# Performance work log

Hardware: AMD Instinct MI355X
Metric: run time of the kernel (lower is better)

## Reference

```python
import jax, jax.numpy as jnp
import numpy as np

BS, NV, BASE_NF = 1, 6890, 13776
NF = 2 * BASE_NF            # fill_back duplicates faces with reversed winding
TS = 3                      # tex_size
IS = 256                    # image_size
NEAR, FAR = 0.1, 100.0
VIEW_ANGLE = 30.0
EYE = np.array([0.0, 0.0, -(1.0 / np.tan(np.radians(VIEW_ANGLE)) + 1.0)], dtype=np.float32)
BG = np.zeros(3, np.float32)               # background_color
AMB_INT, DIR_INT = 1.0, 0.0                # default light settings
AMB_COLOR = np.ones(3, np.float32)
DIR_COLOR = np.ones(3, np.float32)
LIGHT_DIR = np.array([0.0, 1.0, 0.0], np.float32)


def setup_inputs():
    key = jax.random.key(0)
    k1, k2, k3, k4, k5 = jax.random.split(key, 5)
    cam = jnp.concatenate([0.8 + 0.4 * jax.random.uniform(k1, (BS, 1)),
                           0.4 * (jax.random.uniform(k2, (BS, 2)) - 0.5)], axis=-1)
    vertices = 0.5 * jax.random.normal(k3, (BS, NV, 3), dtype=jnp.float32)
    uv_imgs = jax.random.uniform(k4, (BS, 3, IS, IS), dtype=jnp.float32)
    f0 = jax.random.randint(k5, (BASE_NF, 3), 0, NV, dtype=jnp.int32)
    faces = jnp.concatenate([f0, f0[:, ::-1]], axis=0)   # fill_back
    return {"cam": cam, "vertices": vertices, "uv_imgs": uv_imgs, "faces": faces}


def create_coords(ts):
    step = 1.0 / (ts - 1)
    ab = jnp.arange(ts, dtype=jnp.float32) * step
    xv, yv = jnp.meshgrid(ab, ab, indexing='ij')
    return jnp.stack([xv.ravel(), yv.ravel()], axis=0)   # [2, ts*ts]


def grid_sample_bilinear(img, grid):
    # img [B,C,H,W]; grid [B,N,2] with (x,y) in [-1,1]; align_corners=True
    B, C, H, W = img.shape
    x = (grid[..., 0] + 1.0) * 0.5 * (W - 1)
    y = (grid[..., 1] + 1.0) * 0.5 * (H - 1)
    x0 = jnp.floor(x); y0 = jnp.floor(y)
    wx = x - x0; wy = y - y0
    x0i = jnp.clip(x0, 0, W - 1).astype(jnp.int32)
    x1i = jnp.clip(x0 + 1, 0, W - 1).astype(jnp.int32)
    y0i = jnp.clip(y0, 0, H - 1).astype(jnp.int32)
    y1i = jnp.clip(y0 + 1, 0, H - 1).astype(jnp.int32)
    flat = img.reshape(B, C, H * W)
    def g(yi, xi):
        return jnp.take_along_axis(flat, (yi * W + xi)[:, None, :], axis=2)  # [B,C,N]
    return (g(y0i, x0i) * ((1 - wx) * (1 - wy))[:, None]
          + g(y0i, x1i) * (wx * (1 - wy))[:, None]
          + g(y1i, x0i) * ((1 - wx) * wy)[:, None]
          + g(y1i, x1i) * (wx * wy)[:, None])


def dynamic_sampler(cam, vertices, faces, coords):
    # batch_orth_proj_idrot -> points_to_faces -> points_to_sampler
    pts = cam[:, None, 0:1] * (vertices[:, :, :2] + cam[:, None, 1:])  # [B,NV,2]
    fpts = pts[:, faces]                                               # [B,NF,3,2]
    v2 = fpts[:, :, 2]
    m = jnp.stack([fpts[:, :, 0] - v2, fpts[:, :, 1] - v2], axis=-1)   # [B,NF,2,2]
    s = jnp.einsum('bfxk,kt->bfxt', m, coords) + v2[..., None]         # [B,NF,2,T2]
    s = jnp.transpose(s, (0, 1, 3, 2))                                 # [B,NF,T2,2]
    return jnp.clip(s, -1.0, 1.0)


def extract_tex(uv_imgs, sampler):
    B, nf, t2, _ = sampler.shape
    tex = grid_sample_bilinear(uv_imgs, sampler.reshape(B, nf * t2, 2))  # [B,3,NF*T2]
    tex = tex.reshape(B, 3, nf, TS, TS)
    tex = jnp.transpose(tex, (0, 2, 3, 4, 1))                            # [B,NF,T,T,3]
    return jnp.broadcast_to(tex[:, :, :, :, None, :], (B, nf, TS, TS, TS, 3))


def lighting(face_verts, textures):
    v10 = face_verts[:, :, 0] - face_verts[:, :, 1]
    v12 = face_verts[:, :, 2] - face_verts[:, :, 1]
    n = jnp.cross(v10, v12)
    n = n / jnp.maximum(jnp.linalg.norm(n, axis=-1, keepdims=True), 1e-5)
    cos = jnp.maximum(jnp.einsum('bfk,k->bf', n, jnp.asarray(LIGHT_DIR)), 0.0)
    light = AMB_INT * jnp.asarray(AMB_COLOR) + DIR_INT * cos[..., None] * jnp.asarray(DIR_COLOR)
    return textures * light[:, :, None, None, None, :]


def look_at(vertices):
    eye = jnp.asarray(EYE)
    up = jnp.array([0.0, 1.0, 0.0], jnp.float32)
    z = -eye / jnp.linalg.norm(eye)            # at = origin
    x = jnp.cross(up, z); x = x / jnp.linalg.norm(x)
    y = jnp.cross(z, x); y = y / jnp.linalg.norm(y)
    R = jnp.stack([x, y, z], axis=0)
    return (vertices - eye) @ R.T


def rasterize(face_verts, textures):
    # face_verts [B,NF,3,3]: screen x,y in [-1,1], z = depth. textures [B,NF,T,T,T,3].
    B, nf = face_verts.shape[:2]
    fx, fy, fz = face_verts[..., 0], face_verts[..., 1], face_verts[..., 2]
    x0, x1, x2 = fx[..., 0], fx[..., 1], fx[..., 2]
    y0, y1, y2 = fy[..., 0], fy[..., 1], fy[..., 2]
    a = jnp.stack([y1 - y2, y2 - y0, y0 - y1], -1)
    b = jnp.stack([x2 - x1, x0 - x2, x1 - x0], -1)
    c = jnp.stack([x1 * y2 - x2 * y1, x2 * y0 - x0 * y2, x0 * y1 - x1 * y0], -1)
    det = c.sum(-1)
    front = det > 0                                  # backface cull (fill_back handles both sides)
    det_safe = jnp.where(jnp.abs(det) > 1e-10, det, 1e-10)
    fz_safe = jnp.where(jnp.abs(fz) > 1e-6, fz, 1e-6)
    inv_z = 1.0 / fz_safe
    tex_flat = textures.reshape(B, nf * TS * TS * TS, 3)
    xp = (2.0 * jnp.arange(IS, dtype=jnp.float32) + 1.0 - IS) / IS
    yps = (2.0 * jnp.arange(IS, dtype=jnp.float32) + 1.0 - IS) / IS
    bg = jnp.asarray(BG)

    def row_fn(yp):
        # barycentric weights of every pixel in this row against every face
        w = (xp[None, :, None, None] * a[:, None] + yp * b[:, None] + c[:, None]) / det_safe[:, None, :, None]
        inside = (w.min(-1) >= 0.0) & (w.max(-1) <= 1.0) & front[:, None, :]
        den = jnp.sum(w * inv_z[:, None], -1)
        zp = jnp.where(den > 1e-8, 1.0 / jnp.maximum(den, 1e-8), FAR)
        valid = inside & (zp > NEAR) & (zp < FAR)
        depth = jnp.where(valid, zp, FAR)
        fidx = jnp.argmin(depth, axis=2)                                              # [B,W]
        hit = jnp.take_along_axis(depth, fidx[:, :, None], axis=2)[..., 0] < FAR
        w_sel = jnp.take_along_axis(w, fidx[:, :, None, None], axis=2)[:, :, 0, :]    # [B,W,3]
        z_sel = jnp.take_along_axis(fz_safe, fidx[:, :, None], axis=1)                # [B,W,3]
        wc = w_sel / z_sel                                                            # perspective-correct
        wc = wc / jnp.maximum(wc.sum(-1, keepdims=True), 1e-8)
        pos = jnp.clip(wc, 0.0, 1.0) * (TS - 1)
        lo_f = jnp.clip(jnp.floor(pos), 0, TS - 1)
        frac = pos - lo_f
        lo = lo_f.astype(jnp.int32)
        hi = jnp.minimum(lo + 1, TS - 1)
        color = jnp.zeros(w_sel.shape[:2] + (3,), jnp.float32)
        for bits in range(8):                         # trilinear sample of the TxTxT texture cube
            idx = fidx
            wgt = jnp.ones(w_sel.shape[:2], jnp.float32)
            for k in range(3):
                use_hi = (bits >> k) & 1
                ik = hi[..., k] if use_hi else lo[..., k]
                wgt = wgt * (frac[..., k] if use_hi else (1.0 - frac[..., k]))
                idx = idx * TS + ik
            cols = jnp.take_along_axis(tex_flat, idx[:, :, None], axis=1)             # [B,W,3]
            color = color + wgt[..., None] * cols
        return jnp.where(hit[..., None], color, bg)

    row_fn = jax.checkpoint(row_fn)
    def body(carry, yp):
        return carry, row_fn(yp)
    _, rows = jax.lax.scan(body, 0, yps)              # [H,B,W,3]
    return jnp.transpose(rows, (1, 3, 0, 2))          # [B,3,H,W]


def reference(cam, vertices, uv_imgs, faces):
    coords = create_coords(TS)
    sampler = dynamic_sampler(cam, vertices, faces, coords)
    textures = extract_tex(uv_imgs, sampler)
    textures = lighting(vertices[:, faces], textures)
    # orthographic projection (keep z), flip y, then look_at camera transform
    sc = cam[:, 0][:, None, None]
    tr = cam[:, 1:3][:, None, :]
    proj_xy = sc * (vertices[:, :, :2] + tr)
    proj = jnp.concatenate([proj_xy[..., :1], -proj_xy[..., 1:2], vertices[:, :, 2:]], axis=-1)
    v_cam = look_at(proj)
    images = rasterize(v_cam[:, faces], textures)
    return images, textures
```

## Files before the change

kernel.cpp:

```cpp
#include <hip/hip_runtime.h>
#include <hip/hip_bf16.h>

typedef unsigned long long u64;

static constexpr int NF = 27552;
static constexpr int IMGOFF = 3 * 256 * 256;
static constexpr int CAPMAX = 6144;
static constexpr int NWAVES = 8192;

#define EYEZ 2.7320508075688772f

static constexpr size_t OFF_KEYS  = 0;
static constexpr size_t OFF_QTOT  = 524288;
static constexpr size_t OFF_FCNT  = 524292;
static constexpr size_t OFF_CNT   = 524352;
static constexpr size_t OFF_CMETA = 532608;
static constexpr size_t OFF_CF    = 2105472;
static constexpr size_t OFF_CBB   = 3868800;
static constexpr size_t OFF_PXY   = 4309632;
static constexpr size_t OFF_LIST  = 5191296;

static constexpr u64 FARKEY = ((u64)0x42C80000u << 32);

__global__ __launch_bounds__(256) void face_prep(
    const float* __restrict__ cam,
    const float* __restrict__ verts,
    const int* __restrict__ faces,
    u64* __restrict__ keys,
    float* __restrict__ cf,
    float4* __restrict__ cbb,
    float* __restrict__ pxy,
    int* __restrict__ fcnt)
{
    int i = blockIdx.x * 256 + threadIdx.x;
    keys[i] = FARKEY;
    int f = i;
    if (f >= NF) return;
    float c0 = cam[0], c1 = cam[1], c2 = cam[2];
    float z3 = __fdiv_rn(EYEZ, __fsqrt_rn(__fmul_rn(EYEZ, EYEZ)));
    float x0r = __fdiv_rn(z3, __fsqrt_rn(__fmul_rn(z3, z3)));
    float wyy = __fmul_rn(z3, x0r);
    float y1r = __fdiv_rn(wyy, __fsqrt_rn(__fmul_rn(wyy, wyy)));

    float xs[3], ys[3], zs[3], pxv[3], pyv[3];
#pragma unroll
    for (int k = 0; k < 3; k++) {
        int vi = faces[f * 3 + k];
        float vx = verts[vi * 3 + 0];
        float vy = verts[vi * 3 + 1];
        float vz = verts[vi * 3 + 2];
        float px = __fmul_rn(c0, __fadd_rn(vx, c1));
        float py = __fmul_rn(c0, __fadd_rn(vy, c2));
        pxv[k] = px; pyv[k] = py;
        xs[k] = __fmul_rn(px, x0r);
        ys[k] = __fmul_rn(-py, y1r);
        zs[k] = __fmul_rn(__fadd_rn(vz, EYEZ), z3);
    }
    float* pp = pxy + (size_t)f * 8;
    *(float4*)pp = make_float4(pxv[0], pyv[0], pxv[1], pyv[1]);
    *(float2*)(pp + 4) = make_float2(pxv[2], pyv[2]);

    float a0 = __fsub_rn(ys[1], ys[2]);
    float a1 = __fsub_rn(ys[2], ys[0]);
    float a2 = __fsub_rn(ys[0], ys[1]);
    float b0 = __fsub_rn(xs[2], xs[1]);
    float b1 = __fsub_rn(xs[0], xs[2]);
    float b2 = __fsub_rn(xs[1], xs[0]);
    float cc0 = __fsub_rn(__fmul_rn(xs[1], ys[2]), __fmul_rn(xs[2], ys[1]));
    float cc1 = __fsub_rn(__fmul_rn(xs[2], ys[0]), __fmul_rn(xs[0], ys[2]));
    float cc2 = __fsub_rn(__fmul_rn(xs[0], ys[1]), __fmul_rn(xs[1], ys[0]));
    float det = __fadd_rn(__fadd_rn(cc0, cc1), cc2);
    if (det <= 0.0f) return;
    float ds  = (fabsf(det) > 1e-10f) ? det : 1e-10f;
    float z0 = (fabsf(zs[0]) > 1e-6f) ? zs[0] : 1e-6f;
    float z1 = (fabsf(zs[1]) > 1e-6f) ? zs[1] : 1e-6f;
    float z2 = (fabsf(zs[2]) > 1e-6f) ? zs[2] : 1e-6f;
    float iz0 = __fdiv_rn(1.0f, z0);
    float iz1 = __fdiv_rn(1.0f, z1);
    float iz2 = __fdiv_rn(1.0f, z2);

    int pos = atomicAdd(fcnt, 1);
    float* q = cf + (size_t)pos * 16;
    q[0] = a0; q[1] = a1; q[2] = a2;
    q[3] = b0; q[4] = b1; q[5] = b2;
    q[6] = cc0; q[7] = cc1; q[8] = cc2;
    q[9] = ds;
    q[10] = iz0; q[11] = iz1; q[12] = iz2;
    q[13] = 2e-6f * ((iz0 + iz1) + iz2) + 1e-7f;
    q[14] = __int_as_float(f);
    q[15] = fmaxf(fmaxf(iz0, iz1), iz2) * 1.0001f + 1e-7f;

    float4 bb;
    bb.x = fminf(fminf(xs[0], xs[1]), xs[2]) - 1e-4f;
    bb.y = fmaxf(fmaxf(xs[0], xs[1]), xs[2]) + 1e-4f;
    bb.z = fminf(fminf(ys[0], ys[1]), ys[2]) - 1e-4f;
    bb.w = fmaxf(fmaxf(ys[0], ys[1]), ys[2]) + 1e-4f;
    cbb[pos] = bb;
}

__global__ __launch_bounds__(256) void tex_sample(
    const float* __restrict__ pxy,
    const float* __restrict__ uv,
    float* __restrict__ out_tex)
{
    int id = blockIdx.x * 256 + threadIdx.x;
    if (id >= NF * 9) return;
    int f = id / 9, t = id - f * 9;
    const float* pp = pxy + (size_t)f * 8;
    float4 pA = *(const float4*)pp;
    float2 pB = *(const float2*)(pp + 4);
    float px[3] = {pA.x, pA.z, pB.x};
    float py[3] = {pA.y, pA.w, pB.y};
    const float abv[3] = {0.0f, 0.5f, 1.0f};
    int t1 = t / 3, t2 = t - t1 * 3;
    float uu = abv[t1], vv = abv[t2];
    float sx = __fadd_rn(__fadd_rn(__fmul_rn(__fsub_rn(px[0], px[2]), uu),
                                   __fmul_rn(__fsub_rn(px[1], px[2]), vv)), px[2]);
    float sy = __fadd_rn(__fadd_rn(__fmul_rn(__fsub_rn(py[0], py[2]), uu),
                                   __fmul_rn(__fsub_rn(py[1], py[2]), vv)), py[2]);
    sx = fminf(fmaxf(sx, -1.0f), 1.0f);
    sy = fminf(fmaxf(sy, -1.0f), 1.0f);
    float xg = __fmul_rn(__fmul_rn(__fadd_rn(sx, 1.0f), 0.5f), 255.0f);
    float yg = __fmul_rn(__fmul_rn(__fadd_rn(sy, 1.0f), 0.5f), 255.0f);
    float x0f = floorf(xg), y0f = floorf(yg);
    float wx = __fsub_rn(xg, x0f), wy = __fsub_rn(yg, y0f);
    int x0 = (int)x0f; x0 = x0 < 0 ? 0 : (x0 > 255 ? 255 : x0);
    int y0 = (int)y0f; y0 = y0 < 0 ? 0 : (y0 > 255 ? 255 : y0);
    int x1 = x0 + 1 > 255 ? 255 : x0 + 1;
    int y1 = y0 + 1 > 255 ? 255 : y0 + 1;
    float omwx = __fsub_rn(1.0f, wx), omwy = __fsub_rn(1.0f, wy);
    float w00 = __fmul_rn(omwx, omwy);
    float w10 = __fmul_rn(wx, omwy);
    float w01 = __fmul_rn(omwx, wy);
    float w11 = __fmul_rn(wx, wy);
    size_t tb = (size_t)f * 81 + (size_t)t1 * 27 + (size_t)t2 * 9;
#pragma unroll
    for (int c = 0; c < 3; c++) {
        const float* img = uv + c * 65536;
        float g00 = img[y0 * 256 + x0];
        float g10 = img[y0 * 256 + x1];
        float g01 = img[y1 * 256 + x0];
        float g11 = img[y1 * 256 + x1];
        float val = __fmul_rn(g00, w00);
        val = __fadd_rn(val, __fmul_rn(g10, w10));
        val = __fadd_rn(val, __fmul_rn(g01, w01));
        val = __fadd_rn(val, __fmul_rn(g11, w11));
        out_tex[tb + 0 + c] = val;
        out_tex[tb + 3 + c] = val;
        out_tex[tb + 6 + c] = val;
    }
}

__global__ __launch_bounds__(256, 8) void bin_faces(
    const float* __restrict__ cf,
    const float4* __restrict__ cbb,
    const int* __restrict__ fcnt,
    int* __restrict__ cnt,
    int* __restrict__ list,
    int cap)
{
    __shared__ int sfid[4][64];
    const int lane = threadIdx.x & 63;
    const int wid  = threadIdx.x >> 6;
    const int w = blockIdx.x * 4 + wid;
    const int jy = w / 431;
    const int p  = (w - jy * 431) * 64 + lane;
    const int n = *fcnt;
    const float ylo = (float)(16 * jy + 1 - 256) * (1.0f / 256.0f);
    const float yhi = (float)(16 * jy + 15 - 256) * (1.0f / 256.0f);

    bool rv = (p < n);
    float A0 = 0, A1 = 0, A2 = 0, B0 = 0, B1 = 0, B2 = 0;
    int jx0 = 32, jx1 = -1;
    if (rv) {
        float4 bb = cbb[p];
        rv = (yhi >= bb.z) && (ylo <= bb.w);
        if (rv) {
            const float4* q = (const float4*)(cf + (size_t)p * 16);
            float4 q0 = q[0], q1 = q[1], q2 = q[2];
            float a0 = q0.x, a1 = q0.y, a2 = q0.z;
            float b0 = q0.w, b1 = q1.x, b2 = q1.y;
            float c0 = q1.z, c1 = q1.w, c2 = q2.x;
            float K0 = fmaxf(b0 * ylo, b0 * yhi) + c0;
            float K1 = fmaxf(b1 * ylo, b1 * yhi) + c1;
            float K2 = fmaxf(b2 * ylo, b2 * yhi) + c2;
            A0 = a0 * (1.0f / 16.0f);
            A1 = a1 * (1.0f / 16.0f);
            A2 = a2 * (1.0f / 16.0f);
            B0 = a0 * (((a0 > 0.f ? 15.f : 1.f) - 256.f) * (1.0f / 256.0f)) + K0;
            B1 = a1 * (((a1 > 0.f ? 15.f : 1.f) - 256.f) * (1.0f / 256.0f)) + K1;
            B2 = a2 * (((a2 > 0.f ? 15.f : 1.f) - 256.f) * (1.0f / 256.0f)) + K2;
            jx0 = (int)floorf(16.0f * bb.x + 15.0625f);
            jx1 = (int)floorf(16.0f * bb.y + 15.9375f) + 1;
            jx0 = jx0 < 0 ? 0 : jx0;
            jx1 = jx1 > 31 ? 31 : jx1;
        }
    }
    if (__ballot(rv) == 0ull) return;

    sfid[wid][lane] = p;
    asm volatile("s_waitcnt lgkmcnt(0)" ::: "memory");

    u64 mymask = 0;
    for (int jx = 0; jx < 32; jx++) {
        float jf = (float)jx;
        bool pass = rv && (jx >= jx0) && (jx <= jx1) &&
                    (fmaf(jf, A0, B0) >= -1e-3f) &&
                    (fmaf(jf, A1, B1) >= -1e-3f) &&
                    (fmaf(jf, A2, B2) >= -1e-3f);
        u64 mk = __ballot(pass);
        if (lane == jx) mymask = mk;
    }

    int nadd = (lane < 32) ? __popcll(mymask) : 0;
    if (nadd == 0) return;
    int base = atomicAdd(&cnt[jy * 32 + lane], nadd);

    int* dst = list + (size_t)(jy * 32 + lane) * cap;
    u64 mm = mymask;
    int k = 0;
    while (mm) {
        int b = __builtin_ctzll(mm);
        mm &= mm - 1;
        int fid = sfid[wid][b];
        int pos = base + k;
        if (pos < cap) dst[pos] = fid;
        k++;
    }
}

__global__ __launch_bounds__(1024) void prefix_chunks(
    const int* __restrict__ cnt,
    int cap,
    int4* __restrict__ cmeta,
    int* __restrict__ qtot)
{
    __shared__ int hist[128];
    __shared__ int sbase[128];
    __shared__ int bstart[128];
    __shared__ int scat[128];
    const int t = threadIdx.x;
    int len = cnt[t]; if (len > cap) len = cap;
    const int cch = (len + 63) >> 6;
    if (t < 128) hist[t] = 0;
    __syncthreads();
    atomicAdd(&hist[cch], 1);
    __syncthreads();
    if (t == 0) {
        sbase[97] = 0;
        for (int c = 96; c >= 0; c--) sbase[c] = sbase[c + 1] + hist[c + 1];
        int acc = 0;
        for (int j = 0; j <= 96; j++) { bstart[j] = acc; acc += sbase[j]; scat[j] = sbase[j]; }
        *qtot = acc;
    }
    __syncthreads();
    int s = atomicAdd(&scat[cch], 1) - sbase[cch];
    s += 0;
    s += sbase[cch];
    for (int j = 0; j < cch; j++) {
        int m = len - j * 64; if (m > 64) m = 64;
        int4 rec; rec.x = t * cap + j * 64; rec.y = m; rec.z = t; rec.w = 0;
        cmeta[bstart[j] + s] = rec;
    }
}

__global__ __launch_bounds__(256, 8) void raster_score(
    const float* __restrict__ cf,
    const int* __restrict__ list,
    const int4* __restrict__ cmeta,
    const int* __restrict__ qtot,
    u64* __restrict__ keys)
{
    __shared__ __align__(16) float sface[4][1216];
    const int lane = threadIdx.x & 63;
    const int wid  = threadIdx.x >> 6;
    float* sf = sface[wid];
    const int total = *qtot;

    int c = blockIdx.x * 4 + wid;
    if (c >= total) return;
    int4 mt = cmeta[c];

    for (;;) {
        const int4 cur = mt;
        const int cn = c + NWAVES;
        const bool hasnext = (cn < total);
        if (hasnext) mt = cmeta[cn];

        const int tile = cur.z;
        const int m = cur.y;
        const int tx = tile & 31, ty = tile >> 5;
        const int pxi = tx * 8 + (lane & 7), pyi = ty * 8 + (lane >> 3);
        const int pix = pyi * 256 + pxi;
        const float xp = (float)(2 * pxi + 1 - 256) * (1.0f / 256.0f);
        const float yp = (float)(2 * pyi + 1 - 256) * (1.0f / 256.0f);

        float4 g0, g1, g2, g3;
        bool cv = (lane < m);
        if (cv) {
            int cid = list[cur.x + lane];
            const float4* p4 = (const float4*)(cf + (size_t)cid * 16);
            g0 = p4[0]; g1 = p4[1]; g2 = p4[2]; g3 = p4[3];
        }
        u64 sk = keys[pix];
        if (cv) {
            float rds = __builtin_amdgcn_rcpf(g2.y);
            float u0 = g2.z * rds, u1 = g2.w * rds, u2 = g3.x * rds;
            *(float4*)(sf +   0 + lane * 4) = g0;
            *(float4*)(sf + 256 + lane * 4) = g1;
            *(float4*)(sf + 512 + lane * 4) = make_float4(g2.x, u0, u1, u2);
            *(float2*)(sf + 768 + lane * 2) = make_float2(g3.w, g3.y);
            *(float4*)(sf + 896 + lane * 4) = make_float4(g2.y, g2.z, g2.w, g3.x);
            sf[1152 + lane] = g3.z;
        }
        float bfv = __uint_as_float((unsigned)(sk >> 32));
        float thr = fmaxf(0.9935f * __builtin_amdgcn_rcpf(bfv) - 1e-4f, 0.0098f);
        u64 best = FARKEY;
        asm volatile("s_waitcnt lgkmcnt(0)" ::: "memory");

        for (int j = 0; j < m; j++) {
            float2 db = *(const float2*)(sf + 768 + 2 * j);
            if (!__any(db.x >= thr)) continue;
            float4 q0 = *(const float4*)(sf +   0 + 4 * j);
            float4 q1 = *(const float4*)(sf + 256 + 4 * j);
            float4 q2 = *(const float4*)(sf + 512 + 4 * j);
            float t0 = __fadd_rn(__fadd_rn(__fmul_rn(xp, q0.x), __fmul_rn(yp, q0.w)), q1.z);
            float t1 = __fadd_rn(__fadd_rn(__fmul_rn(xp, q0.y), __fmul_rn(yp, q1.x)), q1.w);
            float t2 = __fadd_rn(__fadd_rn(__fmul_rn(xp, q0.z), __fmul_rn(yp, q1.y)), q2.x);
            float tmin = fminf(fminf(t0, t1), t2);
            float dena = fmaf(t0, q2.y, fmaf(t1, q2.z, fmaf(t2, q2.w, db.y)));
            bool pass = (tmin >= 0.0f) && (dena >= thr);
            if (__any(pass)) {
                float4 cc = *(const float4*)(sf + 896 + 4 * j);
                float idb = sf[1152 + j];
                bool in = !(t0 < 0.0f) && !(t1 < 0.0f) && !(t2 < 0.0f);
                float w0 = __fdiv_rn(t0, cc.x);
                float w1 = __fdiv_rn(t1, cc.x);
                float w2 = __fdiv_rn(t2, cc.x);
                in = in && !(w0 > 1.0f) && !(w1 > 1.0f) && !(w2 > 1.0f);
                float den = __fmul_rn(w0, cc.y);
                den = __fadd_rn(den, __fmul_rn(w1, cc.z));
                den = __fadd_rn(den, __fmul_rn(w2, cc.w));
                if (in && den > 1e-8f) {
                    float zp = __fdiv_rn(1.0f, den);
                    if (zp > 0.1f && zp < 100.0f) {
                        u64 key = ((u64)__float_as_uint(zp) << 32)
                                | (u64)(unsigned)__float_as_int(idb);
                        if (key < best) {
                            best = key;
                            float b2f = __uint_as_float((unsigned)(best >> 32));
                            thr = fmaxf(thr,
                                0.9935f * __builtin_amdgcn_rcpf(b2f) - 1e-4f);
                        }
                    }
                }
            }
        }
        if (best != FARKEY)
            atomicMin(&keys[pix], best);
        if (!hasnext) return;
        c = cn;
    }
}

__global__ __launch_bounds__(256) void epilogue(
    const u64* __restrict__ keys,
    const float* __restrict__ cam,
    const float* __restrict__ verts,
    const int* __restrict__ faces,
    const float* __restrict__ tex,
    float* __restrict__ out_img)
{
    int pix = blockIdx.x * 256 + threadIdx.x;
    int xo = pix & 255, yo = pix >> 8;
    const float xp = (float)(2 * xo + 1 - 256) * (1.0f / 256.0f);
    const float yp = (float)(2 * yo + 1 - 256) * (1.0f / 256.0f);
    u64 m = keys[pix];
    float depth = __uint_as_float((unsigned)(m >> 32));
    float col0 = 0.f, col1 = 0.f, col2 = 0.f;
    if (depth < 100.0f) {
        int fidx = (int)(unsigned)(m & 0xFFFFFFFFu);
        float c0 = cam[0], c1 = cam[1], c2 = cam[2];
        float z3 = __fdiv_rn(EYEZ, __fsqrt_rn(__fmul_rn(EYEZ, EYEZ)));
        float x0r = __fdiv_rn(z3, __fsqrt_rn(__fmul_rn(z3, z3)));
        float wyy = __fmul_rn(z3, x0r);
        float y1r = __fdiv_rn(wyy, __fsqrt_rn(__fmul_rn(wyy, wyy)));
        float xs[3], ys[3], zs[3];
#pragma unroll
        for (int i = 0; i < 3; i++) {
            int vi = faces[fidx * 3 + i];
            float vx = verts[vi * 3 + 0];
            float vy = verts[vi * 3 + 1];
            float vz = verts[vi * 3 + 2];
            float px = __fmul_rn(c0, __fadd_rn(vx, c1));
            float py = __fmul_rn(c0, __fadd_rn(vy, c2));
            xs[i] = __fmul_rn(px, x0r);
            ys[i] = __fmul_rn(-py, y1r);
            zs[i] = __fmul_rn(__fadd_rn(vz, EYEZ), z3);
        }
        float a0 = __fsub_rn(ys[1], ys[2]);
        float a1 = __fsub_rn(ys[2], ys[0]);
        float a2 = __fsub_rn(ys[0], ys[1]);
        float b0 = __fsub_rn(xs[2], xs[1]);
        float b1 = __fsub_rn(xs[0], xs[2]);
        float b2 = __fsub_rn(xs[1], xs[0]);
        float cc0 = __fsub_rn(__fmul_rn(xs[1], ys[2]), __fmul_rn(xs[2], ys[1]));
        float cc1 = __fsub_rn(__fmul_rn(xs[2], ys[0]), __fmul_rn(xs[0], ys[2]));
        float cc2 = __fsub_rn(__fmul_rn(xs[0], ys[1]), __fmul_rn(xs[1], ys[0]));
        float det = __fadd_rn(__fadd_rn(cc0, cc1), cc2);
        float dsf = (fabsf(det) > 1e-10f) ? det : 1e-10f;
        float z0 = (fabsf(zs[0]) > 1e-6f) ? zs[0] : 1e-6f;
        float z1 = (fabsf(zs[1]) > 1e-6f) ? zs[1] : 1e-6f;
        float z2 = (fabsf(zs[2]) > 1e-6f) ? zs[2] : 1e-6f;

        float t0 = __fadd_rn(__fadd_rn(__fmul_rn(xp, a0), __fmul_rn(yp, b0)), cc0);
        float t1 = __fadd_rn(__fadd_rn(__fmul_rn(xp, a1), __fmul_rn(yp, b1)), cc1);
        float t2 = __fadd_rn(__fadd_rn(__fmul_rn(xp, a2), __fmul_rn(yp, b2)), cc2);
        float w0 = __fdiv_rn(t0, dsf), w1 = __fdiv_rn(t1, dsf), w2 = __fdiv_rn(t2, dsf);
        float wc0 = __fdiv_rn(w0, z0);
        float wc1 = __fdiv_rn(w1, z1);
        float wc2 = __fdiv_rn(w2, z2);
        float ssum = __fadd_rn(__fadd_rn(wc0, wc1), wc2);
        float dnm = fmaxf(ssum, 1e-8f);
        wc0 = __fdiv_rn(wc0, dnm); wc1 = __fdiv_rn(wc1, dnm); wc2 = __fdiv_rn(wc2, dnm);
        float pos0 = __fmul_rn(fminf(fmaxf(wc0, 0.f), 1.f), 2.0f);
        float pos1 = __fmul_rn(fminf(fmaxf(wc1, 0.f), 1.f), 2.0f);
        float pos2 = __fmul_rn(fminf(fmaxf(wc2, 0.f), 1.f), 2.0f);
        float lf0 = fminf(fmaxf(floorf(pos0), 0.f), 2.f);
        float lf1 = fminf(fmaxf(floorf(pos1), 0.f), 2.f);
        float lf2 = fminf(fmaxf(floorf(pos2), 0.f), 2.f);
        float fr0 = __fsub_rn(pos0, lf0), fr1 = __fsub_rn(pos1, lf1), fr2 = __fsub_rn(pos2, lf2);
        int lo0 = (int)lf0, lo1 = (int)lf1;
        int hi0 = lo0 + 1 > 2 ? 2 : lo0 + 1;
        int hi1 = lo1 + 1 > 2 ? 2 : lo1 + 1;
        const float* tbase = tex + (size_t)fidx * 81;
#pragma unroll
        for (int bits = 0; bits < 8; bits++) {
            int u0 = bits & 1, u1 = (bits >> 1) & 1, u2 = (bits >> 2) & 1;
            int i0 = u0 ? hi0 : lo0;
            int i1 = u1 ? hi1 : lo1;
            float e0 = u0 ? fr0 : __fsub_rn(1.0f, fr0);
            float e1 = u1 ? fr1 : __fsub_rn(1.0f, fr1);
            float e2 = u2 ? fr2 : __fsub_rn(1.0f, fr2);
            float wgt = __fmul_rn(__fmul_rn(e0, e1), e2);
            const float* tp = tbase + (size_t)i0 * 27 + (size_t)i1 * 9;
            col0 = __fadd_rn(col0, __fmul_rn(wgt, tp[0]));
            col1 = __fadd_rn(col1, __fmul_rn(wgt, tp[1]));
            col2 = __fadd_rn(col2, __fmul_rn(wgt, tp[2]));
        }
    }
    out_img[pix]          = col0;
    out_img[65536 + pix]  = col1;
    out_img[131072 + pix] = col2;
}

extern "C" void kernel_launch(void* const* d_in, const int* in_sizes, int n_in,
                              void* d_out, int out_size, void* d_ws, size_t ws_size,
                              hipStream_t stream) {
    const float* cam   = (const float*)d_in[0];
    const float* verts = (const float*)d_in[1];
    const float* uv    = (const float*)d_in[2];
    const int*   faces = (const int*)d_in[3];
    float* out = (float*)d_out;

    char* ws = (char*)d_ws;
    u64*    keys  = (u64*)(ws + OFF_KEYS);
    int*    qtot  = (int*)(ws + OFF_QTOT);
    int*    fcnt  = (int*)(ws + OFF_FCNT);
    int*    cntp  = (int*)(ws + OFF_CNT);
    int4*   cmeta = (int4*)(ws + OFF_CMETA);
    float*  cf    = (float*)(ws + OFF_CF);
    float4* cbb   = (float4*)(ws + OFF_CBB);
    float*  pxy   = (float*)(ws + OFF_PXY);
    int*    list  = (int*)(ws + OFF_LIST);

    int cap = CAPMAX;
    if (ws_size > OFF_LIST) {
        size_t avail = (ws_size - OFF_LIST) / (1024 * sizeof(int));
        if ((size_t)cap > avail) cap = (int)avail;
    } else {
        cap = 0;
    }

    float* out_img = out;
    float* out_tex = out + IMGOFF;

    hipMemsetAsync(ws + OFF_QTOT, 0, (OFF_CNT + 4096) - OFF_QTOT, stream);

    hipLaunchKernelGGL(face_prep, dim3(256), dim3(256), 0, stream,
                       cam, verts, faces, keys, cf, cbb, pxy, fcnt);
    hipLaunchKernelGGL(tex_sample, dim3((NF * 9 + 255) / 256), dim3(256), 0, stream,
                       pxy, uv, out_tex);
    hipLaunchKernelGGL(bin_faces, dim3(3448), dim3(256), 0, stream,
                       cf, cbb, fcnt, cntp, list, cap);
    hipLaunchKernelGGL(prefix_chunks, dim3(1), dim3(1024), 0, stream,
                       cntp, cap, cmeta, qtot);
    hipLaunchKernelGGL(raster_score, dim3(NWAVES / 4), dim3(256), 0, stream,
                       cf, list, cmeta, qtot, keys);
    hipLaunchKernelGGL(epilogue, dim3(256), dim3(256), 0, stream,
                       keys, cam, verts, faces, out_tex, out_img);
}
```

Baseline: 153.0 us.

## Fuse face prep and texture sampling into one kernel, drop memset and compaction

Merges the face setup and texture sampling kernels into one prep kernel, where one of every nine threads per face also computes the edge coefficients and bounding box. The memset is removed: keys and bin counters are now zeroed inside the prep kernel. The atomic compaction of front-facing faces is replaced by direct indexing by face id, with back-facing faces given an empty bounding box. This saves two launches, the intermediate pxy buffer and the atomic counter, but the binning kernel now scans all faces, including culled ones.

```diff
diff --git a/kernel.cpp b/kernel.cpp
--- a/kernel.cpp
+++ b/kernel.cpp
@@ -12,105 +12,41 @@
 
 static constexpr size_t OFF_KEYS  = 0;
 static constexpr size_t OFF_QTOT  = 524288;
-static constexpr size_t OFF_FCNT  = 524292;
 static constexpr size_t OFF_CNT   = 524352;
 static constexpr size_t OFF_CMETA = 532608;
 static constexpr size_t OFF_CF    = 2105472;
 static constexpr size_t OFF_CBB   = 3868800;
-static constexpr size_t OFF_PXY   = 4309632;
-static constexpr size_t OFF_LIST  = 5191296;
+static constexpr size_t OFF_LIST  = 4309632;
 
 static constexpr u64 FARKEY = ((u64)0x42C80000u << 32);
 
-__global__ __launch_bounds__(256) void face_prep(
+__global__ __launch_bounds__(256) void prep(
     const float* __restrict__ cam,
     const float* __restrict__ verts,
     const int* __restrict__ faces,
+    const float* __restrict__ uv,
     u64* __restrict__ keys,
+    int* __restrict__ cnt,
     float* __restrict__ cf,
     float4* __restrict__ cbb,
-    float* __restrict__ pxy,
-    int* __restrict__ fcnt)
+    float* __restrict__ out_tex)
 {
     int i = blockIdx.x * 256 + threadIdx.x;
-    keys[i] = FARKEY;
-    int f = i;
-    if (f >= NF) return;
+    if (i < 65536) keys[i] = FARKEY;
+    if (i < 1024) cnt[i] = 0;
+    if (i >= NF * 9) return;
+    int f = i / 9, t = i - f * 9;
     float c0 = cam[0], c1 = cam[1], c2 = cam[2];
-    float z3 = __fdiv_rn(EYEZ, __fsqrt_rn(__fmul_rn(EYEZ, EYEZ)));
-    float x0r = __fdiv_rn(z3, __fsqrt_rn(__fmul_rn(z3, z3)));
-    float wyy = __fmul_rn(z3, x0r);
-    float y1r = __fdiv_rn(wyy, __fsqrt_rn(__fmul_rn(wyy, wyy)));
-
-    float xs[3], ys[3], zs[3], pxv[3], pyv[3];
-#pragma unroll
-    for (int k = 0; k < 3; k++) {
-        int vi = faces[f * 3 + k];
-        float vx = verts[vi * 3 + 0];
-        float vy = verts[vi * 3 + 1];
-        float vz = verts[vi * 3 + 2];
-        float px = __fmul_rn(c0, __fadd_rn(vx, c1));
-        float py = __fmul_rn(c0, __fadd_rn(vy, c2));
-        pxv[k] = px; pyv[k] = py;
-        xs[k] = __fmul_rn(px, x0r);
-        ys[k] = __fmul_rn(-py, y1r);
-        zs[k] = __fmul_rn(__fadd_rn(vz, EYEZ), z3);
-    }
-    float* pp = pxy + (size_t)f * 8;
-    *(float4*)pp = make_float4(pxv[0], pyv[0], pxv[1], pyv[1]);
-    *(float2*)(pp + 4) = make_float2(pxv[2], pyv[2]);
-
-    float a0 = __fsub_rn(ys[1], ys[2]);
-    float a1 = __fsub_rn(ys[2], ys[0]);
-    float a2 = __fsub_rn(ys[0], ys[1]);
-    float b0 = __fsub_rn(xs[2], xs[1]);
-    float b1 = __fsub_rn(xs[0], xs[2]);
-    float b2 = __fsub_rn(xs[1], xs[0]);
-    float cc0 = __fsub_rn(__fmul_rn(xs[1], ys[2]), __fmul_rn(xs[2], ys[1]));
-    float cc1 = __fsub_rn(__fmul_rn(xs[2], ys[0]), __fmul_rn(xs[0], ys[2]));
-    float cc2 = __fsub_rn(__fmul_rn(xs[0], ys[1]), __fmul_rn(xs[1], ys[0]));
-    float det = __fadd_rn(__fadd_rn(cc0, cc1), cc2);
-    if (det <= 0.0f) return;
-    float ds  = (fabsf(det) > 1e-10f) ? det : 1e-10f;
-    float z0 = (fabsf(zs[0]) > 1e-6f) ? zs[0] : 1e-6f;
-    float z1 = (fabsf(zs[1]) > 1e-6f) ? zs[1] : 1e-6f;
-    float z2 = (fabsf(zs[2]) > 1e-6f) ? zs[2] : 1e-6f;
-    float iz0 = __fdiv_rn(1.0f, z0);
-    float iz1 = __fdiv_rn(1.0f, z1);
-    float iz2 = __fdiv_rn(1.0f, z2);
-
-    int pos = atomicAdd(fcnt, 1);
-    float* q = cf + (size_t)pos * 16;
-    q[0] = a0; q[1] = a1; q[2] = a2;
-    q[3] = b0; q[4] = b1; q[5] = b2;
-    q[6] = cc0; q[7] = cc1; q[8] = cc2;
-    q[9] = ds;
-    q[10] = iz0; q[11] = iz1; q[12] = iz2;
-    q[13] = 2e-6f * ((iz0 + iz1) + iz2) + 1e-7f;
-    q[14] = __int_as_float(f);
-    q[15] = fmaxf(fmaxf(iz0, iz1), iz2) * 1.0001f + 1e-7f;
-
-    float4 bb;
-    bb.x = fminf(fminf(xs[0], xs[1]), xs[2]) - 1e-4f;
-    bb.y = fmaxf(fmaxf(xs[0], xs[1]), xs[2]) + 1e-4f;
-    bb.z = fminf(fminf(ys[0], ys[1]), ys[2]) - 1e-4f;
-    bb.w = fmaxf(fmaxf(ys[0], ys[1]), ys[2]) + 1e-4f;
-    cbb[pos] = bb;
-}
-
-__global__ __launch_bounds__(256) void tex_sample(
-    const float* __restrict__ pxy,
-    const float* __restrict__ uv,
-    float* __restrict__ out_tex)
-{
-    int id = blockIdx.x * 256 + threadIdx.x;
-    if (id >= NF * 9) return;
-    int f = id / 9, t = id - f * 9;
-    const float* pp = pxy + (size_t)f * 8;
-    float4 pA = *(const float4*)pp;
-    float2 pB = *(const float2*)(pp + 4);
-    float px[3] = {pA.x, pA.z, pB.x};
-    float py[3] = {pA.y, pA.w, pB.y};
+
+    int vi0 = faces[f * 3 + 0], vi1 = faces[f * 3 + 1], vi2 = faces[f * 3 + 2];
+    float px[3], py[3];
+    px[0] = __fmul_rn(c0, __fadd_rn(verts[vi0 * 3 + 0], c1));
+    py[0] = __fmul_rn(c0, __fadd_rn(verts[vi0 * 3 + 1], c2));
+    px[1] = __fmul_rn(c0, __fadd_rn(verts[vi1 * 3 + 0], c1));
+    py[1] = __fmul_rn(c0, __fadd_rn(verts[vi1 * 3 + 1], c2));
+    px[2] = __fmul_rn(c0, __fadd_rn(verts[vi2 * 3 + 0], c1));
+    py[2] = __fmul_rn(c0, __fadd_rn(verts[vi2 * 3 + 1], c2));
+
     const float abv[3] = {0.0f, 0.5f, 1.0f};
     int t1 = t / 3, t2 = t - t1 * 3;
     float uu = abv[t1], vv = abv[t2];
@@ -149,12 +85,64 @@
         out_tex[tb + 3 + c] = val;
         out_tex[tb + 6 + c] = val;
     }
+
+    if (t != 0) return;
+    float z3 = __fdiv_rn(EYEZ, __fsqrt_rn(__fmul_rn(EYEZ, EYEZ)));
+    float x0r = __fdiv_rn(z3, __fsqrt_rn(__fmul_rn(z3, z3)));
+    float wyy = __fmul_rn(z3, x0r);
+    float y1r = __fdiv_rn(wyy, __fsqrt_rn(__fmul_rn(wyy, wyy)));
+    float xs[3], ys[3], zs[3];
+    int vis[3] = {vi0, vi1, vi2};
+#pragma unroll
+    for (int k = 0; k < 3; k++) {
+        xs[k] = __fmul_rn(px[k], x0r);
+        ys[k] = __fmul_rn(-py[k], y1r);
+        zs[k] = __fmul_rn(__fadd_rn(verts[vis[k] * 3 + 2], EYEZ), z3);
+    }
+    float a0 = __fsub_rn(ys[1], ys[2]);
+    float a1 = __fsub_rn(ys[2], ys[0]);
+    float a2 = __fsub_rn(ys[0], ys[1]);
+    float b0 = __fsub_rn(xs[2], xs[1]);
+    float b1 = __fsub_rn(xs[0], xs[2]);
+    float b2 = __fsub_rn(xs[1], xs[0]);
+    float cc0 = __fsub_rn(__fmul_rn(xs[1], ys[2]), __fmul_rn(xs[2], ys[1]));
+    float cc1 = __fsub_rn(__fmul_rn(xs[2], ys[0]), __fmul_rn(xs[0], ys[2]));
+    float cc2 = __fsub_rn(__fmul_rn(xs[0], ys[1]), __fmul_rn(xs[1], ys[0]));
+    float det = __fadd_rn(__fadd_rn(cc0, cc1), cc2);
+    if (det <= 0.0f) {
+        float4 bb; bb.x = 3e30f; bb.y = -3e30f; bb.z = 3e30f; bb.w = -3e30f;
+        cbb[f] = bb;
+        return;
+    }
+    float ds  = (fabsf(det) > 1e-10f) ? det : 1e-10f;
+    float z0 = (fabsf(zs[0]) > 1e-6f) ? zs[0] : 1e-6f;
+    float z1 = (fabsf(zs[1]) > 1e-6f) ? zs[1] : 1e-6f;
+    float z2 = (fabsf(zs[2]) > 1e-6f) ? zs[2] : 1e-6f;
+    float iz0 = __fdiv_rn(1.0f, z0);
+    float iz1 = __fdiv_rn(1.0f, z1);
+    float iz2 = __fdiv_rn(1.0f, z2);
+
+    float* q = cf + (size_t)f * 16;
+    q[0] = a0; q[1] = a1; q[2] = a2;
+    q[3] = b0; q[4] = b1; q[5] = b2;
+    q[6] = cc0; q[7] = cc1; q[8] = cc2;
+    q[9] = ds;
+    q[10] = iz0; q[11] = iz1; q[12] = iz2;
+    q[13] = 2e-6f * ((iz0 + iz1) + iz2) + 1e-7f;
+    q[14] = __int_as_float(f);
+    q[15] = fmaxf(fmaxf(iz0, iz1), iz2) * 1.0001f + 1e-7f;
+
+    float4 bb;
+    bb.x = fminf(fminf(xs[0], xs[1]), xs[2]) - 1e-4f;
+    bb.y = fmaxf(fmaxf(xs[0], xs[1]), xs[2]) + 1e-4f;
+    bb.z = fminf(fminf(ys[0], ys[1]), ys[2]) - 1e-4f;
+    bb.w = fmaxf(fmaxf(ys[0], ys[1]), ys[2]) + 1e-4f;
+    cbb[f] = bb;
 }
 
 __global__ __launch_bounds__(256, 8) void bin_faces(
     const float* __restrict__ cf,
     const float4* __restrict__ cbb,
-    const int* __restrict__ fcnt,
     int* __restrict__ cnt,
     int* __restrict__ list,
     int cap)
@@ -165,11 +153,10 @@
     const int w = blockIdx.x * 4 + wid;
     const int jy = w / 431;
     const int p  = (w - jy * 431) * 64 + lane;
-    const int n = *fcnt;
     const float ylo = (float)(16 * jy + 1 - 256) * (1.0f / 256.0f);
     const float yhi = (float)(16 * jy + 15 - 256) * (1.0f / 256.0f);
 
-    bool rv = (p < n);
+    bool rv = (p < NF);
     float A0 = 0, A1 = 0, A2 = 0, B0 = 0, B1 = 0, B2 = 0;
     int jx0 = 32, jx1 = -1;
     if (rv) {
@@ -254,9 +241,7 @@
         *qtot = acc;
     }
     __syncthreads();
-    int s = atomicAdd(&scat[cch], 1) - sbase[cch];
-    s += 0;
-    s += sbase[cch];
+    int s = atomicAdd(&scat[cch], 1);
     for (int j = 0; j < cch; j++) {
         int m = len - j * 64; if (m > 64) m = 64;
         int4 rec; rec.x = t * cap + j * 64; rec.y = m; rec.z = t; rec.w = 0;
@@ -466,12 +451,10 @@
     char* ws = (char*)d_ws;
     u64*    keys  = (u64*)(ws + OFF_KEYS);
     int*    qtot  = (int*)(ws + OFF_QTOT);
-    int*    fcnt  = (int*)(ws + OFF_FCNT);
     int*    cntp  = (int*)(ws + OFF_CNT);
     int4*   cmeta = (int4*)(ws + OFF_CMETA);
     float*  cf    = (float*)(ws + OFF_CF);
     float4* cbb   = (float4*)(ws + OFF_CBB);
-    float*  pxy   = (float*)(ws + OFF_PXY);
     int*    list  = (int*)(ws + OFF_LIST);
 
     int cap = CAPMAX;
@@ -485,14 +468,10 @@
     float* out_img = out;
     float* out_tex = out + IMGOFF;
 
-    hipMemsetAsync(ws + OFF_QTOT, 0, (OFF_CNT + 4096) - OFF_QTOT, stream);
-
-    hipLaunchKernelGGL(face_prep, dim3(256), dim3(256), 0, stream,
-                       cam, verts, faces, keys, cf, cbb, pxy, fcnt);
-    hipLaunchKernelGGL(tex_sample, dim3((NF * 9 + 255) / 256), dim3(256), 0, stream,
-                       pxy, uv, out_tex);
+    hipLaunchKernelGGL(prep, dim3((NF * 9 + 255) / 256), dim3(256), 0, stream,
+                       cam, verts, faces, uv, keys, cntp, cf, cbb, out_tex);
     hipLaunchKernelGGL(bin_faces, dim3(3448), dim3(256), 0, stream,
-                       cf, cbb, fcnt, cntp, list, cap);
+                       cf, cbb, cntp, list, cap);
     hipLaunchKernelGGL(prefix_chunks, dim3(1), dim3(1024), 0, stream,
                        cntp, cap, cmeta, qtot);
     hipLaunchKernelGGL(raster_score, dim3(NWAVES / 4), dim3(256), 0, stream,
```

Result: slower. 159.4 us (+4.2%).
